# Kernel optimization log

Hardware: AMD Instinct MI355X
Metric: run time of the kernel (lower is better)

The kernel has to match this reference:

```python
import jax, jax.numpy as jnp
import numpy as np

CODEBOOK_SIZE = 8192
D_LATENT = 512
COMMITMENT_COST = 0.25


def setup_inputs() -> dict:
    key = jax.random.key(0)
    k1, k2 = jax.random.split(key)
    z = jax.random.normal(k1, (4, 2048, D_LATENT), dtype=jnp.float32)
    # embedding initialized uniform(-1/K, 1/K) in the original; scale a normal draw similarly
    W = jax.random.uniform(k2, (CODEBOOK_SIZE, D_LATENT), dtype=jnp.float32,
                           minval=-1.0 / CODEBOOK_SIZE, maxval=1.0 / CODEBOOK_SIZE)
    return {"z": z, "W": W}


def reference(z, W):
    # Eval-mode forward (no EMA buffer mutation): quantize, straight-through, losses.
    B, S, D = z.shape
    K = W.shape[0]
    z_flat = z.reshape(-1, D)  # [N, D]

    # squared-euclidean distances: ||z||^2 - 2 z W^T + ||w||^2  -> [N, K]
    distances = (jnp.sum(z_flat * z_flat, axis=-1, keepdims=True)
                 - 2.0 * (z_flat @ W.T)
                 + jnp.sum(W * W, axis=-1))
    indices = jnp.argmin(distances, axis=-1)  # [N] int
    z_q = W[indices]  # [N, D] gather

    commitment_loss = jnp.mean((z_flat - jax.lax.stop_gradient(z_q)) ** 2)

    # straight-through estimator
    quantized = z_flat + jax.lax.stop_gradient(z_q - z_flat)

    # perplexity over codebook usage
    counts = jnp.zeros((K,), dtype=jnp.float32).at[indices].add(1.0)
    avg_probs = counts / z_flat.shape[0]
    perplexity = jnp.exp(-jnp.sum(avg_probs * jnp.log(avg_probs + 1e-10)))

    quantized = quantized.reshape(B, S, D)
    indices = indices.reshape(B, S)
    return (quantized, indices, COMMITMENT_COST * commitment_loss, perplexity)
```

## Files before the change

### kernel.cpp

```cpp
#include <hip/hip_runtime.h>
#include <math.h>


typedef __attribute__((ext_vector_type(8))) _Float16 f16x8;
typedef __attribute__((ext_vector_type(16))) float f32x16;

constexpr int N_ROWS = 8192;
constexpr int K_CODES = 8192;
constexpr int D_DIM = 512;
constexpr float COMMIT = 0.25f;
constexpr float EPS = 3.0e-4f;

constexpr size_t OFF_LOSS    = 0;
constexpr size_t OFF_COUNTS  = 64;
constexpr size_t OFF_PARTIAL = 8256;
constexpr size_t OFF_ZZ      = 16384;
constexpr size_t OFF_WW      = 24576;
constexpr size_t OFF_BESTD   = 32768;
constexpr size_t OFF_BESTI   = 2129920;
constexpr size_t F16_BASE_BYTES = 16908288;
constexpr size_t SPLIT_ELEMS = (size_t)8192 * 512;
constexpr size_t SPLIT_BYTES = SPLIT_ELEMS * 2;
constexpr size_t WS_NEED = F16_BASE_BYTES + 2 * SPLIT_BYTES;

constexpr int SPLITK = 8;
constexpr int KSPL = K_CODES / SPLITK;

#define MFMA16(a, b, c) __builtin_amdgcn_mfma_f32_32x32x16_f16((a), (b), (c), 0, 0, 0)

__global__ __launch_bounds__(256) void rowss_kernel(const float* __restrict__ src,
                                                    float* __restrict__ dst) {
  int row  = (blockIdx.x * 256 + threadIdx.x) >> 6;
  int lane = threadIdx.x & 63;
  const float* p = src + (size_t)row * D_DIM;
  float4 a = *(const float4*)&p[lane * 4];
  float4 b = *(const float4*)&p[256 + lane * 4];
  float s = a.x*a.x + a.y*a.y + a.z*a.z + a.w*a.w
          + b.x*b.x + b.y*b.y + b.z*b.z + b.w*b.w;
#pragma unroll
  for (int off = 32; off > 0; off >>= 1) s += __shfl_down(s, off, 64);
  if (lane == 0) dst[row] = s;
}

__global__ __launch_bounds__(256) void split_hi_kernel(const float* __restrict__ src,
                                                       unsigned short* __restrict__ hi,
                                                       float scale) {
  const int dt = blockIdx.x;
  const int rb = blockIdx.y;
  const int t = threadIdx.x;
  const int row = t >> 1;
  const int dh = (t & 1) * 16;
  const float* sp = src + ((size_t)(rb * 128 + row)) * D_DIM + dt * 32 + dh;
  const float4* sp4 = (const float4*)sp;
  float4 va = sp4[0], vb = sp4[1], vc = sp4[2], vd = sp4[3];
  float v[16] = {va.x, va.y, va.z, va.w, vb.x, vb.y, vb.z, vb.w,
                 vc.x, vc.y, vc.z, vc.w, vd.x, vd.y, vd.z, vd.w};
  const size_t tile = (size_t)(rb * 16 + dt) * 4096;
#pragma unroll
  for (int c2 = 0; c2 < 2; c2++) {
    const int chunk = (t & 1) * 2 + c2;
    f16x8 hv;
#pragma unroll
    for (int j = 0; j < 8; j++) hv[j] = (_Float16)(v[c2 * 8 + j] * scale);
    *(f16x8*)(hi + tile + (size_t)chunk * 1024 + (size_t)row * 8) = hv;
  }
}

__global__ __launch_bounds__(256, 3) void vq_screen_kernel(
    const unsigned short* __restrict__ zh_s, const unsigned short* __restrict__ wh_s,
    const float* __restrict__ ww,
    float* __restrict__ bestd2, int* __restrict__ besti2) {
  const int tid = threadIdx.x;
  const int cb = blockIdx.x, rb = blockIdx.y;
  const int lane = tid & 63, wv = tid >> 6;
  const int wr = wv >> 1, wc = wv & 1;
  const int lrow = lane & 31, lhi = lane >> 5;

  const f16x8* zh8 = (const f16x8*)zh_s;
  const f16x8* wh8 = (const f16x8*)wh_s;

  f32x16 acc[2][2];
#pragma unroll
  for (int i = 0; i < 2; i++)
#pragma unroll
    for (int j = 0; j < 2; j++)
#pragma unroll
      for (int e = 0; e < 16; e++) acc[i][j][e] = 0.0f;

  const int wbase = wr * 64 + lrow;
  const int zbase = wc * 64 + lrow;

#pragma unroll 2
  for (int dt = 0; dt < 16; dt++) {
    const int wt = (cb * 16 + dt) * 512;
    const int zt = (rb * 16 + dt) * 512;
    f16x8 wf[2][2], zf[2][2];
#pragma unroll
    for (int ks = 0; ks < 2; ks++) {
      const int ch = ks * 2 + lhi;
      wf[ks][0] = wh8[wt + ch * 128 + wbase];
      wf[ks][1] = wh8[wt + ch * 128 + wbase + 32];
      zf[ks][0] = zh8[zt + ch * 128 + zbase];
      zf[ks][1] = zh8[zt + ch * 128 + zbase + 32];
    }
    __builtin_amdgcn_s_setprio(1);
#pragma unroll
    for (int ks = 0; ks < 2; ks++) {
      acc[0][0] = MFMA16(wf[ks][0], zf[ks][0], acc[0][0]);
      acc[0][1] = MFMA16(wf[ks][0], zf[ks][1], acc[0][1]);
      acc[1][0] = MFMA16(wf[ks][1], zf[ks][0], acc[1][0]);
      acc[1][1] = MFMA16(wf[ks][1], zf[ks][1], acc[1][1]);
    }
    __builtin_amdgcn_s_setprio(0);
  }

#pragma unroll
  for (int cf = 0; cf < 2; cf++) {
    float p1d = 3.4e38f, p2d = 3.4e38f;
    int   p1i = 0x7fffffff, p2i = 0x7fffffff;
#pragma unroll
    for (int rf = 0; rf < 2; rf++) {
      const int cbase = cb * 128 + wr * 64 + rf * 32 + 4 * lhi;
#pragma unroll
      for (int reg = 0; reg < 16; reg++) {
        const int ci = cbase + (reg & 3) + 8 * (reg >> 2);
        const float d = fmaf(acc[rf][cf][reg], -2.44140625e-4f, ww[ci]);
        const bool b1 = d < p1d;
        const bool b2 = d < p2d;
        p2d = b1 ? p1d : (b2 ? d : p2d);
        p2i = b1 ? p1i : (b2 ? ci : p2i);
        p1d = b1 ? d : p1d;
        p1i = b1 ? ci : p1i;
      }
    }
    const float q1d = __shfl_xor(p1d, 32, 64); const int q1i = __shfl_xor(p1i, 32, 64);
    const float q2d = __shfl_xor(p2d, 32, 64); const int q2i = __shfl_xor(p2i, 32, 64);
    float t1d, t2d; int t1i, t2i;
    if (q1d < p1d) {
      t1d = q1d; t1i = q1i;
      if (p1d < q2d) { t2d = p1d; t2i = p1i; } else { t2d = q2d; t2i = q2i; }
    } else {
      t1d = p1d; t1i = p1i;
      if (q1d < p2d) { t2d = q1d; t2i = q1i; } else { t2d = p2d; t2i = p2i; }
    }
    if (lhi == 0) {
      const int row = rb * 128 + wc * 64 + cf * 32 + lrow;
      const size_t o = (size_t)row * 256 + (size_t)(cb * 2 + wr) * 2;
      float2 dv2; dv2.x = t1d; dv2.y = t2d;
      int2   iv2; iv2.x = t1i; iv2.y = t2i;
      *(float2*)&bestd2[o] = dv2;
      *(int2*)&besti2[o]   = iv2;
    }
  }
}

__global__ __launch_bounds__(256) void vq_rescore_kernel(
    const float* __restrict__ z, const float* __restrict__ W,
    const float* __restrict__ zz, const float* __restrict__ ww,
    const float* __restrict__ bestd2, const int* __restrict__ besti2,
    float* __restrict__ out, float* __restrict__ ws_f) {
  const int row  = (blockIdx.x * 256 + threadIdx.x) >> 6;
  const int lane = threadIdx.x & 63;
  const size_t base = (size_t)row * 256;
  const float4 dv = *(const float4*)&bestd2[base + lane * 4];
  const int4  iv = *(const int4*)&besti2[base + lane * 4];
  float dd[4] = {dv.x, dv.y, dv.z, dv.w};
  int   ii[4] = {iv.x, iv.y, iv.z, iv.w};

  float m = fminf(fminf(dd[0], dd[1]), fminf(dd[2], dd[3]));
#pragma unroll
  for (int mm = 1; mm <= 32; mm <<= 1) m = fminf(m, __shfl_xor(m, mm, 64));
  const float thr = m + EPS;

  const float* zp = z + (size_t)row * D_DIM;
  const float4 za = *(const float4*)&zp[lane * 8];
  const float4 zb = *(const float4*)&zp[lane * 8 + 4];
  const float zzr = zz[row];

  float bd = 3.4e38f; int bi = 0x7fffffff;
#pragma unroll
  for (int s = 0; s < 4; s++) {
    unsigned long long mset = __ballot(dd[s] <= thr);
    while (mset) {
      const int b = __ffsll((long long)mset) - 1;
      mset &= mset - 1;
      const int c = __shfl(ii[s], b, 64);
      const float* wp = W + (size_t)c * D_DIM;
      const float4 wa = *(const float4*)&wp[lane * 8];
      const float4 wb = *(const float4*)&wp[lane * 8 + 4];
      float dot = za.x*wa.x + za.y*wa.y + za.z*wa.z + za.w*wa.w
                + zb.x*wb.x + zb.y*wb.y + zb.z*wb.z + zb.w*wb.w;
#pragma unroll
      for (int mm = 1; mm <= 32; mm <<= 1) dot += __shfl_xor(dot, mm, 64);
      const float dist = (zzr - 2.0f * dot) + ww[c];
      if (dist < bd || (dist == bd && c < bi)) { bd = dist; bi = c; }
    }
  }

  if (lane == 0) {
    out[(size_t)N_ROWS * D_DIM + row] = (float)bi;
    atomicAdd(&ws_f[OFF_COUNTS + bi], 1.0f);
  }
  const float* wp = W + (size_t)bi * D_DIM;
  float* op = out + (size_t)row * D_DIM;
  float lsum = 0.f;
#pragma unroll
  for (int h = 0; h < 2; h++) {
    const int dd2 = h * 256 + lane * 4;
    const float4 zv = *(const float4*)&zp[dd2];
    const float4 wv = *(const float4*)&wp[dd2];
    float4 q;
    q.x = zv.x + (wv.x - zv.x);
    q.y = zv.y + (wv.y - zv.y);
    q.z = zv.z + (wv.z - zv.z);
    q.w = zv.w + (wv.w - zv.w);
    *(float4*)&op[dd2] = q;
    float dx;
    dx = zv.x - wv.x; lsum += dx * dx;
    dx = zv.y - wv.y; lsum += dx * dx;
    dx = zv.z - wv.z; lsum += dx * dx;
    dx = zv.w - wv.w; lsum += dx * dx;
  }
#pragma unroll
  for (int off = 32; off > 0; off >>= 1) lsum += __shfl_down(lsum, off, 64);
  __shared__ float lred[4];
  if (lane == 0) lred[threadIdx.x >> 6] = lsum;
  __syncthreads();
  if (threadIdx.x == 0)
    ws_f[OFF_PARTIAL + blockIdx.x] = lred[0] + lred[1] + lred[2] + lred[3];
}

constexpr int BN = 64, BK = 64, BD = 32;
__global__ __launch_bounds__(256) void vq_dist_kernel(
    const float* __restrict__ z, const float* __restrict__ W,
    const float* __restrict__ zz, const float* __restrict__ ww,
    float* __restrict__ bestd_out, int* __restrict__ besti_out) {
  __shared__ float zs[BD][68];
  __shared__ float ws_[BD][68];
  __shared__ float rd[BN][16];
  __shared__ int   ri[BN][16];
  const int tid = threadIdx.x;
  const int tx = tid & 15;
  const int ty = tid >> 4;
  const int r0 = blockIdx.x * BN;
  const int kbase0 = blockIdx.y * KSPL;
  const int lr = tid >> 3;
  const int lc = tid & 7;
  float bd[4]; int bi[4];
#pragma unroll
  for (int i = 0; i < 4; i++) { bd[i] = 3.4e38f; bi[i] = 0x7fffffff; }
  float zzr[4];
#pragma unroll
  for (int i = 0; i < 4; i++) zzr[i] = zz[r0 + ty * 4 + i];
  for (int kt = 0; kt < KSPL; kt += BK) {
    const int kb = kbase0 + kt;
    float c[4][4];
#pragma unroll
    for (int i = 0; i < 4; i++)
#pragma unroll
      for (int j = 0; j < 4; j++) c[i][j] = 0.f;
    for (int dtt = 0; dtt < D_DIM; dtt += BD) {
#pragma unroll
      for (int h = 0; h < 2; h++) {
        const int r = lr + h * 32;
        const float4 v = *(const float4*)&z[(size_t)(r0 + r) * D_DIM + dtt + lc * 4];
        zs[lc*4+0][r] = v.x; zs[lc*4+1][r] = v.y; zs[lc*4+2][r] = v.z; zs[lc*4+3][r] = v.w;
        const float4 u = *(const float4*)&W[(size_t)(kb + r) * D_DIM + dtt + lc * 4];
        ws_[lc*4+0][r] = u.x; ws_[lc*4+1][r] = u.y; ws_[lc*4+2][r] = u.z; ws_[lc*4+3][r] = u.w;
      }
      __syncthreads();
#pragma unroll
      for (int d = 0; d < BD; d++) {
        const float4 a = *(const float4*)&zs[d][ty * 4];
        const float4 b = *(const float4*)&ws_[d][tx * 4];
        c[0][0] += a.x*b.x; c[0][1] += a.x*b.y; c[0][2] += a.x*b.z; c[0][3] += a.x*b.w;
        c[1][0] += a.y*b.x; c[1][1] += a.y*b.y; c[1][2] += a.y*b.z; c[1][3] += a.y*b.w;
        c[2][0] += a.z*b.x; c[2][1] += a.z*b.y; c[2][2] += a.z*b.z; c[2][3] += a.z*b.w;
        c[3][0] += a.w*b.x; c[3][1] += a.w*b.y; c[3][2] += a.w*b.z; c[3][3] += a.w*b.w;
      }
      __syncthreads();
    }
#pragma unroll
    for (int i = 0; i < 4; i++) {
#pragma unroll
      for (int j = 0; j < 4; j++) {
        const int col = kb + tx * 4 + j;
        const float dist = (zzr[i] - 2.0f * c[i][j]) + ww[col];
        if (dist < bd[i]) { bd[i] = dist; bi[i] = col; }
      }
    }
  }
#pragma unroll
  for (int i = 0; i < 4; i++) { rd[ty * 4 + i][tx] = bd[i]; ri[ty * 4 + i][tx] = bi[i]; }
  __syncthreads();
  if (tid < BN) {
    float best = rd[tid][0]; int bidx = ri[tid][0];
#pragma unroll
    for (int t = 1; t < 16; t++) {
      const float dv = rd[tid][t]; const int iv = ri[tid][t];
      if (dv < best || (dv == best && iv < bidx)) { best = dv; bidx = iv; }
    }
    bestd_out[(size_t)blockIdx.y * N_ROWS + r0 + tid] = best;
    besti_out[(size_t)blockIdx.y * N_ROWS + r0 + tid] = bidx;
  }
}

__global__ __launch_bounds__(256) void vq_gather8_kernel(
    const float* __restrict__ z, const float* __restrict__ W,
    const float* __restrict__ bestd, const int* __restrict__ besti,
    float* __restrict__ out, float* __restrict__ ws_f) {
  const int row  = (blockIdx.x * 256 + threadIdx.x) >> 6;
  const int lane = threadIdx.x & 63;
  int bidx = 0;
  if (lane == 0) {
    float best = bestd[row];
    bidx = besti[row];
#pragma unroll
    for (int s = 1; s < SPLITK; s++) {
      const float dv = bestd[(size_t)s * N_ROWS + row];
      const int iv = besti[(size_t)s * N_ROWS + row];
      if (dv < best || (dv == best && iv < bidx)) { best = dv; bidx = iv; }
    }
    out[(size_t)N_ROWS * D_DIM + row] = (float)bidx;
    atomicAdd(&ws_f[OFF_COUNTS + bidx], 1.0f);
  }
  bidx = __shfl(bidx, 0, 64);
  const float* zp = z + (size_t)row * D_DIM;
  const float* wp = W + (size_t)bidx * D_DIM;
  float* op = out + (size_t)row * D_DIM;
  float lsum = 0.f;
#pragma unroll
  for (int h = 0; h < 2; h++) {
    const int d = h * 256 + lane * 4;
    const float4 zv = *(const float4*)&zp[d];
    const float4 wv = *(const float4*)&wp[d];
    float4 q;
    q.x = zv.x + (wv.x - zv.x);
    q.y = zv.y + (wv.y - zv.y);
    q.z = zv.z + (wv.z - zv.z);
    q.w = zv.w + (wv.w - zv.w);
    *(float4*)&op[d] = q;
    float dx;
    dx = zv.x - wv.x; lsum += dx * dx;
    dx = zv.y - wv.y; lsum += dx * dx;
    dx = zv.z - wv.z; lsum += dx * dx;
    dx = zv.w - wv.w; lsum += dx * dx;
  }
#pragma unroll
  for (int off = 32; off > 0; off >>= 1) lsum += __shfl_down(lsum, off, 64);
  if (lane == 0) atomicAdd(&ws_f[OFF_LOSS], lsum);
}

__global__ __launch_bounds__(256) void vq_finalize_kernel(const float* __restrict__ ws_f,
                                                          float* __restrict__ out,
                                                          int use_partial) {
  const int tid = threadIdx.x;
  float ls = 0.f;
  if (use_partial) {
    for (int i = tid; i < 2048; i += 256) ls += ws_f[OFF_PARTIAL + i];
  }
  float s = 0.f;
  for (int k = tid; k < K_CODES; k += 256) {
    const float p = ws_f[OFF_COUNTS + k] * (1.0f / 8192.0f);
    s += p * logf(p + 1e-10f);
  }
#pragma unroll
  for (int off = 32; off > 0; off >>= 1) {
    s  += __shfl_down(s, off, 64);
    ls += __shfl_down(ls, off, 64);
  }
  __shared__ float red[4], redl[4];
  if ((tid & 63) == 0) { red[tid >> 6] = s; redl[tid >> 6] = ls; }
  __syncthreads();
  if (tid == 0) {
    const float tot = red[0] + red[1] + red[2] + red[3];
    const float L = use_partial ? (redl[0] + redl[1] + redl[2] + redl[3])
                                : ws_f[OFF_LOSS];
    out[(size_t)N_ROWS * D_DIM + N_ROWS]     = COMMIT * (L / 4194304.0f);
    out[(size_t)N_ROWS * D_DIM + N_ROWS + 1] = expf(-tot);
  }
}

extern "C" void kernel_launch(void* const* d_in, const int* in_sizes, int n_in,
                              void* d_out, int out_size, void* d_ws, size_t ws_size,
                              hipStream_t stream) {
  const float* z = (const float*)d_in[0];
  const float* W = (const float*)d_in[1];
  float* out = (float*)d_out;
  float* ws_f = (float*)d_ws;
  int* ws_i = (int*)d_ws;

  hipMemsetAsync(d_ws, 0, (OFF_COUNTS + K_CODES) * sizeof(float), stream);

  rowss_kernel<<<N_ROWS / 4, 256, 0, stream>>>(z, ws_f + OFF_ZZ);
  rowss_kernel<<<K_CODES / 4, 256, 0, stream>>>(W, ws_f + OFF_WW);

  if (ws_size >= WS_NEED) {
    unsigned short* zh = (unsigned short*)((char*)d_ws + F16_BASE_BYTES);
    unsigned short* wh = zh + SPLIT_ELEMS;
    split_hi_kernel<<<dim3(16, 64), 256, 0, stream>>>(z, zh, 1.0f);
    split_hi_kernel<<<dim3(16, 64), 256, 0, stream>>>(W, wh, 8192.0f);
    vq_screen_kernel<<<dim3(64, 64), 256, 0, stream>>>(
        zh, wh, ws_f + OFF_WW, ws_f + OFF_BESTD, ws_i + OFF_BESTI);
    vq_rescore_kernel<<<N_ROWS / 4, 256, 0, stream>>>(
        z, W, ws_f + OFF_ZZ, ws_f + OFF_WW,
        ws_f + OFF_BESTD, ws_i + OFF_BESTI, out, ws_f);
    vq_finalize_kernel<<<1, 256, 0, stream>>>(ws_f, out, 1);
  } else {
    dim3 grid(N_ROWS / BN, SPLITK);
    vq_dist_kernel<<<grid, 256, 0, stream>>>(z, W, ws_f + OFF_ZZ, ws_f + OFF_WW,
                                             ws_f + OFF_BESTD, ws_i + OFF_BESTI);
    vq_gather8_kernel<<<N_ROWS / 4, 256, 0, stream>>>(z, W, ws_f + OFF_BESTD,
                                                      ws_i + OFF_BESTI, out, ws_f);
    vq_finalize_kernel<<<1, 256, 0, stream>>>(ws_f, out, 0);
  }
}
```

Baseline: 216.8 us.

## Fuse prep kernels, double-buffer screen loads, and remap blocks for XCD locality

Replaces the memset, two row-norm kernels and two fp16 split kernels with one prep kernel that zeroes the counters, computes row norms and writes the tiled fp16 copies in a single pass. The screen GEMM kernel now double-buffers its fragment loads across d-tiles, and it uses a 1D grid with a block index swizzle that groups blocks sharing z and W tiles onto the same XCD for L2 reuse. Occupancy is lowered to 2 blocks per CU to make room for the extra registers. This cuts launch overhead and global reads in the prep stage and hides load latency in the GEMM, at the cost of fewer waves resident per CU to hide latency.

```diff
diff --git a/kernel.cpp b/kernel.cpp
--- a/kernel.cpp
+++ b/kernel.cpp
@@ -28,91 +28,121 @@
 
 #define MFMA16(a, b, c) __builtin_amdgcn_mfma_f32_32x32x16_f16((a), (b), (c), 0, 0, 0)
 
-__global__ __launch_bounds__(256) void rowss_kernel(const float* __restrict__ src,
-                                                    float* __restrict__ dst) {
-  int row  = (blockIdx.x * 256 + threadIdx.x) >> 6;
-  int lane = threadIdx.x & 63;
-  const float* p = src + (size_t)row * D_DIM;
-  float4 a = *(const float4*)&p[lane * 4];
-  float4 b = *(const float4*)&p[256 + lane * 4];
-  float s = a.x*a.x + a.y*a.y + a.z*a.z + a.w*a.w
-          + b.x*b.x + b.y*b.y + b.z*b.z + b.w*b.w;
-#pragma unroll
-  for (int off = 32; off > 0; off >>= 1) s += __shfl_down(s, off, 64);
-  if (lane == 0) dst[row] = s;
-}
-
-__global__ __launch_bounds__(256) void split_hi_kernel(const float* __restrict__ src,
-                                                       unsigned short* __restrict__ hi,
-                                                       float scale) {
-  const int dt = blockIdx.x;
-  const int rb = blockIdx.y;
-  const int t = threadIdx.x;
-  const int row = t >> 1;
-  const int dh = (t & 1) * 16;
-  const float* sp = src + ((size_t)(rb * 128 + row)) * D_DIM + dt * 32 + dh;
-  const float4* sp4 = (const float4*)sp;
-  float4 va = sp4[0], vb = sp4[1], vc = sp4[2], vd = sp4[3];
-  float v[16] = {va.x, va.y, va.z, va.w, vb.x, vb.y, vb.z, vb.w,
-                 vc.x, vc.y, vc.z, vc.w, vd.x, vd.y, vd.z, vd.w};
-  const size_t tile = (size_t)(rb * 16 + dt) * 4096;
-#pragma unroll
-  for (int c2 = 0; c2 < 2; c2++) {
-    const int chunk = (t & 1) * 2 + c2;
+__device__ __forceinline__ bool lexless(float da, int ia, float db, int ib) {
+  return da < db || (da == db && ia < ib);
+}
+
+__global__ __launch_bounds__(256) void prep_kernel(
+    const float* __restrict__ z, const float* __restrict__ W,
+    unsigned short* __restrict__ zh, unsigned short* __restrict__ wh,
+    float* __restrict__ ws_f) {
+  const int src = blockIdx.y;
+  const int tid = threadIdx.x;
+  if (src == 0 && blockIdx.x < 11) {
+#pragma unroll
+    for (int k = 0; k < 4; k++) {
+      const int idx = blockIdx.x * 1024 + k * 256 + tid;
+      if (idx < 10304) ws_f[idx] = 0.0f;
+    }
+  }
+  const float* S = src ? W : z;
+  unsigned short* H = src ? wh : zh;
+  const float scale = src ? 8192.0f : 1.0f;
+  float* norm = ws_f + (src ? OFF_WW : OFF_ZZ);
+
+  const int row = blockIdx.x * 64 + (tid >> 2);
+  const int q = tid & 3;
+  const float* sp = S + (size_t)row * D_DIM + q * 128;
+  const size_t tbase = (size_t)(row >> 7) * 16 * 4096 + (size_t)(row & 127) * 8;
+
+  float4 ssv = {0.f, 0.f, 0.f, 0.f};
+#pragma unroll
+  for (int c = 0; c < 16; c++) {
+    const float4 x = *(const float4*)&sp[c * 8];
+    const float4 y = *(const float4*)&sp[c * 8 + 4];
+    ssv.x += x.x * x.x; ssv.y += x.y * x.y; ssv.z += x.z * x.z; ssv.w += x.w * x.w;
+    ssv.x += y.x * y.x; ssv.y += y.y * y.y; ssv.z += y.z * y.z; ssv.w += y.w * y.w;
     f16x8 hv;
-#pragma unroll
-    for (int j = 0; j < 8; j++) hv[j] = (_Float16)(v[c2 * 8 + j] * scale);
-    *(f16x8*)(hi + tile + (size_t)chunk * 1024 + (size_t)row * 8) = hv;
-  }
-}
-
-__global__ __launch_bounds__(256, 3) void vq_screen_kernel(
+    hv[0] = (_Float16)(x.x * scale); hv[1] = (_Float16)(x.y * scale);
+    hv[2] = (_Float16)(x.z * scale); hv[3] = (_Float16)(x.w * scale);
+    hv[4] = (_Float16)(y.x * scale); hv[5] = (_Float16)(y.y * scale);
+    hv[6] = (_Float16)(y.z * scale); hv[7] = (_Float16)(y.w * scale);
+    const int d = q * 128 + c * 8;
+    const int dt = d >> 5;
+    const int chunk = (d >> 3) & 3;
+    *(f16x8*)&H[tbase + (size_t)dt * 4096 + (size_t)chunk * 1024] = hv;
+  }
+  float s = (ssv.x + ssv.y) + (ssv.z + ssv.w);
+  s += __shfl_xor(s, 1, 64);
+  s += __shfl_xor(s, 2, 64);
+  if (q == 0) norm[row] = s;
+}
+
+__global__ __launch_bounds__(256, 2) void vq_screen_kernel(
     const unsigned short* __restrict__ zh_s, const unsigned short* __restrict__ wh_s,
     const float* __restrict__ ww,
     float* __restrict__ bestd2, int* __restrict__ besti2) {
   const int tid = threadIdx.x;
-  const int cb = blockIdx.x, rb = blockIdx.y;
+  const int bid = blockIdx.x;
+  const int xcd = bid & 7;
+  const int j = bid >> 3;
+  const int stid = xcd * 8 + (j >> 6);
+  const int wi = j & 63;
+  const int cb = (stid & 7) * 8 + (wi & 7);
+  const int rb = (stid >> 3) * 8 + (wi >> 3);
+
   const int lane = tid & 63, wv = tid >> 6;
   const int wr = wv >> 1, wc = wv & 1;
   const int lrow = lane & 31, lhi = lane >> 5;
 
   const f16x8* zh8 = (const f16x8*)zh_s;
   const f16x8* wh8 = (const f16x8*)wh_s;
-
-  f32x16 acc[2][2];
-#pragma unroll
-  for (int i = 0; i < 2; i++)
-#pragma unroll
-    for (int j = 0; j < 2; j++)
-#pragma unroll
-      for (int e = 0; e < 16; e++) acc[i][j][e] = 0.0f;
-
   const int wbase = wr * 64 + lrow;
   const int zbase = wc * 64 + lrow;
 
-#pragma unroll 2
-  for (int dt = 0; dt < 16; dt++) {
-    const int wt = (cb * 16 + dt) * 512;
-    const int zt = (rb * 16 + dt) * 512;
-    f16x8 wf[2][2], zf[2][2];
-#pragma unroll
-    for (int ks = 0; ks < 2; ks++) {
-      const int ch = ks * 2 + lhi;
-      wf[ks][0] = wh8[wt + ch * 128 + wbase];
-      wf[ks][1] = wh8[wt + ch * 128 + wbase + 32];
-      zf[ks][0] = zh8[zt + ch * 128 + zbase];
-      zf[ks][1] = zh8[zt + ch * 128 + zbase + 32];
-    }
-    __builtin_amdgcn_s_setprio(1);
-#pragma unroll
-    for (int ks = 0; ks < 2; ks++) {
-      acc[0][0] = MFMA16(wf[ks][0], zf[ks][0], acc[0][0]);
-      acc[0][1] = MFMA16(wf[ks][0], zf[ks][1], acc[0][1]);
-      acc[1][0] = MFMA16(wf[ks][1], zf[ks][0], acc[1][0]);
-      acc[1][1] = MFMA16(wf[ks][1], zf[ks][1], acc[1][1]);
-    }
-    __builtin_amdgcn_s_setprio(0);
-  }
+  f32x16 acc[2][2];
+#pragma unroll
+  for (int i = 0; i < 2; i++)
+#pragma unroll
+    for (int jj = 0; jj < 2; jj++)
+#pragma unroll
+      for (int e = 0; e < 16; e++) acc[i][jj][e] = 0.0f;
+
+  f16x8 wA[4], zA[4], wB[4], zB[4];
+
+#define LOADB(WX, ZX, dt) { \
+    const int wt_ = (cb * 16 + (dt)) * 512; \
+    const int zt_ = (rb * 16 + (dt)) * 512; \
+    _Pragma("unroll") \
+    for (int ks = 0; ks < 2; ks++) { \
+      const int ch_ = ks * 2 + lhi; \
+      WX[ks*2+0] = wh8[wt_ + ch_*128 + wbase]; \
+      WX[ks*2+1] = wh8[wt_ + ch_*128 + wbase + 32]; \
+      ZX[ks*2+0] = zh8[zt_ + ch_*128 + zbase]; \
+      ZX[ks*2+1] = zh8[zt_ + ch_*128 + zbase + 32]; \
+    } }
+
+#define COMPUTEB(WX, ZX) { \
+    __builtin_amdgcn_s_setprio(1); \
+    _Pragma("unroll") \
+    for (int ks = 0; ks < 2; ks++) { \
+      acc[0][0] = MFMA16(WX[ks*2+0], ZX[ks*2+0], acc[0][0]); \
+      acc[0][1] = MFMA16(WX[ks*2+0], ZX[ks*2+1], acc[0][1]); \
+      acc[1][0] = MFMA16(WX[ks*2+1], ZX[ks*2+0], acc[1][0]); \
+      acc[1][1] = MFMA16(WX[ks*2+1], ZX[ks*2+1], acc[1][1]); \
+    } \
+    __builtin_amdgcn_s_setprio(0); }
+
+  LOADB(wA, zA, 0);
+#pragma unroll
+  for (int dtp = 0; dtp < 8; dtp++) {
+    LOADB(wB, zB, dtp * 2 + 1);
+    COMPUTEB(wA, zA);
+    if (dtp < 7) LOADB(wA, zA, dtp * 2 + 2);
+    COMPUTEB(wB, zB);
+  }
+#undef LOADB
+#undef COMPUTEB
 
 #pragma unroll
   for (int cf = 0; cf < 2; cf++) {
@@ -228,6 +258,20 @@
   __syncthreads();
   if (threadIdx.x == 0)
     ws_f[OFF_PARTIAL + blockIdx.x] = lred[0] + lred[1] + lred[2] + lred[3];
+}
+
+__global__ __launch_bounds__(256) void rowss_kernel(const float* __restrict__ src,
+                                                    float* __restrict__ dst) {
+  int row  = (blockIdx.x * 256 + threadIdx.x) >> 6;
+  int lane = threadIdx.x & 63;
+  const float* p = src + (size_t)row * D_DIM;
+  float4 a = *(const float4*)&p[lane * 4];
+  float4 b = *(const float4*)&p[256 + lane * 4];
+  float s = a.x*a.x + a.y*a.y + a.z*a.z + a.w*a.w
+          + b.x*b.x + b.y*b.y + b.z*b.z + b.w*b.w;
+#pragma unroll
+  for (int off = 32; off > 0; off >>= 1) s += __shfl_down(s, off, 64);
+  if (lane == 0) dst[row] = s;
 }
 
 constexpr int BN = 64, BK = 64, BD = 32;
@@ -258,7 +302,7 @@
 #pragma unroll
     for (int i = 0; i < 4; i++)
 #pragma unroll
-      for (int j = 0; j < 4; j++) c[i][j] = 0.f;
+      for (int jj = 0; jj < 4; jj++) c[i][jj] = 0.f;
     for (int dtt = 0; dtt < D_DIM; dtt += BD) {
 #pragma unroll
       for (int h = 0; h < 2; h++) {
@@ -283,9 +327,9 @@
 #pragma unroll
     for (int i = 0; i < 4; i++) {
 #pragma unroll
-      for (int j = 0; j < 4; j++) {
-        const int col = kb + tx * 4 + j;
-        const float dist = (zzr[i] - 2.0f * c[i][j]) + ww[col];
+      for (int jj = 0; jj < 4; jj++) {
+        const int col = kb + tx * 4 + jj;
+        const float dist = (zzr[i] - 2.0f * c[i][jj]) + ww[col];
         if (dist < bd[i]) { bd[i] = dist; bi[i] = col; }
       }
     }
@@ -390,23 +434,20 @@
   float* ws_f = (float*)d_ws;
   int* ws_i = (int*)d_ws;
 
-  hipMemsetAsync(d_ws, 0, (OFF_COUNTS + K_CODES) * sizeof(float), stream);
-
-  rowss_kernel<<<N_ROWS / 4, 256, 0, stream>>>(z, ws_f + OFF_ZZ);
-  rowss_kernel<<<K_CODES / 4, 256, 0, stream>>>(W, ws_f + OFF_WW);
-
   if (ws_size >= WS_NEED) {
     unsigned short* zh = (unsigned short*)((char*)d_ws + F16_BASE_BYTES);
     unsigned short* wh = zh + SPLIT_ELEMS;
-    split_hi_kernel<<<dim3(16, 64), 256, 0, stream>>>(z, zh, 1.0f);
-    split_hi_kernel<<<dim3(16, 64), 256, 0, stream>>>(W, wh, 8192.0f);
-    vq_screen_kernel<<<dim3(64, 64), 256, 0, stream>>>(
+    prep_kernel<<<dim3(128, 2), 256, 0, stream>>>(z, W, zh, wh, ws_f);
+    vq_screen_kernel<<<4096, 256, 0, stream>>>(
         zh, wh, ws_f + OFF_WW, ws_f + OFF_BESTD, ws_i + OFF_BESTI);
     vq_rescore_kernel<<<N_ROWS / 4, 256, 0, stream>>>(
         z, W, ws_f + OFF_ZZ, ws_f + OFF_WW,
         ws_f + OFF_BESTD, ws_i + OFF_BESTI, out, ws_f);
     vq_finalize_kernel<<<1, 256, 0, stream>>>(ws_f, out, 1);
   } else {
+    hipMemsetAsync(d_ws, 0, (OFF_COUNTS + K_CODES) * sizeof(float), stream);
+    rowss_kernel<<<N_ROWS / 4, 256, 0, stream>>>(z, ws_f + OFF_ZZ);
+    rowss_kernel<<<K_CODES / 4, 256, 0, stream>>>(W, ws_f + OFF_WW);
     dim3 grid(N_ROWS / BN, SPLITK);
     vq_dist_kernel<<<grid, 256, 0, stream>>>(z, W, ws_f + OFF_ZZ, ws_f + OFF_WW,
                                              ws_f + OFF_BESTD, ws_i + OFF_BESTI);
```

After: 216.7 us. About the same (-0.1%).
